# Performance work log

Hardware: AMD Instinct MI355X
Metric: run time of the kernel (lower is better)

## Reference

```python
import jax, jax.numpy as jnp
import numpy as np

B, S, D = 8, 2048, 1024  # batch, seq_len, d_model == output_size


def setup_inputs() -> dict:
    key = jax.random.key(0)
    ks = jax.random.split(key, 10)
    scale = 1.0 / np.sqrt(D)
    return {
        "query": jax.random.normal(ks[0], (B, S, D), jnp.float32),
        "key": jax.random.normal(ks[1], (B, S, D), jnp.float32),
        "value": jax.random.normal(ks[2], (B, S, D), jnp.float32),
        "mask": jax.random.randint(ks[3], (B, S), 0, 2, jnp.int32),
        "Wq": jax.random.uniform(ks[4], (D, D), jnp.float32, -scale, scale),
        "bq": jax.random.uniform(ks[5], (D,), jnp.float32, -scale, scale),
        "Wk": jax.random.uniform(ks[6], (D, D), jnp.float32, -scale, scale),
        "bk": jax.random.uniform(ks[7], (D,), jnp.float32, -scale, scale),
        "Wv": jax.random.uniform(ks[8], (D, D), jnp.float32, -scale, scale),
        "bv": jax.random.uniform(ks[9], (D,), jnp.float32, -scale, scale),
    }


def reference(query, key, value, mask, Wq, bq, Wk, bk, Wv, bv):
    # Linear projections (torch Linear: x @ W.T + b)
    Q = jnp.einsum("bsd,od->bso", query, Wq) + bq
    K = jnp.einsum("bsd,od->bso", key, Wk) + bk
    V = jnp.einsum("bsd,od->bso", value, Wv) + bv
    d_k = K.shape[-1]
    scores = jnp.einsum("bqd,bkd->bqk", Q, K) / jnp.sqrt(jnp.float32(d_k))
    # 2-D mask [B, S_k] -> broadcast over query positions; masked_fill(~mask, -inf)
    m = (mask != 0)[:, None, :]  # [B, 1, S_k]
    scores = jnp.where(m, scores, -jnp.inf)
    weights = jax.nn.softmax(scores, axis=-1)
    # dropout omitted (eval-mode / deterministic baseline)
    out = jnp.einsum("bqk,bkv->bqv", weights, V)
    return out
```

## Files before the change

### kernel.cpp

```cpp
#include <hip/hip_runtime.h>


#define BATCH 8
#define SEQ   2048
#define DM    1024

typedef __bf16 bf16x8 __attribute__((ext_vector_type(8)));
typedef float  f32x4  __attribute__((ext_vector_type(4)));
typedef unsigned short ushort8 __attribute__((ext_vector_type(8)));
typedef unsigned short ushort4v __attribute__((ext_vector_type(4)));

__device__ __forceinline__ unsigned short f2b(float f) {
    __bf16 h = (__bf16)f;
    return __builtin_bit_cast(unsigned short, h);
}

__device__ __forceinline__ void stage_async(const unsigned short* g,
                                            unsigned short* l) {
    __builtin_amdgcn_global_load_lds(
        (const __attribute__((address_space(1))) void*)g,
        (__attribute__((address_space(3))) void*)l, 16, 0, 0);
}

__device__ __forceinline__ void frag_mfma48(const unsigned short* As,
                                            const unsigned short* Bs,
                                            f32x4 acc[4][8], int waveM,
                                            int waveN, int quad, int l16) {
    bf16x8 af[4], bf[8];
#pragma unroll
    for (int i = 0; i < 4; ++i)
        af[i] = *(const bf16x8*)(As + (waveM * 64 + i * 16 + l16) * 32 + quad * 8);
#pragma unroll
    for (int j = 0; j < 8; ++j)
        bf[j] = *(const bf16x8*)(Bs + (waveN * 128 + j * 16 + l16) * 32 + quad * 8);
#pragma unroll
    for (int i = 0; i < 4; ++i)
#pragma unroll
        for (int j = 0; j < 8; ++j)
            acc[i][j] = __builtin_amdgcn_mfma_f32_16x16x32_bf16(
                af[i], bf[j], acc[i][j], 0, 0, 0);
}

__global__ __launch_bounds__(256) void build_idx(
    const int* __restrict__ mask, int* __restrict__ idx,
    int* __restrict__ cnt, int* __restrict__ cntp) {
    const int b = blockIdx.x;
    const int* m = mask + b * SEQ;
    const int t = threadIdx.x;
    __shared__ int sums[256];
    int loc[8], s = 0;
#pragma unroll
    for (int u = 0; u < 8; ++u) { loc[u] = (m[t * 8 + u] != 0); s += loc[u]; }
    sums[t] = s;
    __syncthreads();
    for (int off = 1; off < 256; off <<= 1) {
        int v = (t >= off) ? sums[t - off] : 0;
        __syncthreads();
        sums[t] += v;
        __syncthreads();
    }
    int base = sums[t] - s;
#pragma unroll
    for (int u = 0; u < 8; ++u)
        if (loc[u]) idx[b * SEQ + base++] = t * 8 + u;
    if (t == 255) {
        cnt[b] = sums[255];
        cntp[b] = (sums[255] + 127) & ~127;
    }
}

__global__ void cast_bf16_all(const float* __restrict__ Wq,
                              const float* __restrict__ Wk,
                              const float* __restrict__ Wv,
                              unsigned short* __restrict__ wq,
                              unsigned short* __restrict__ wk,
                              unsigned short* __restrict__ wv) {
    const int p = blockIdx.x >> 9;
    const int lb = blockIdx.x & 511;
    const float* src = (p == 0) ? Wq : (p == 1) ? Wk : Wv;
    unsigned short* dst = (p == 0) ? wq : (p == 1) ? wk : wv;
    int i = lb * blockDim.x + threadIdx.x;
    const f32x4* s4 = (const f32x4*)src;
    f32x4 a = s4[2 * i], b = s4[2 * i + 1];
    ushort8 o;
    o[0] = f2b(a[0]); o[1] = f2b(a[1]); o[2] = f2b(a[2]); o[3] = f2b(a[3]);
    o[4] = f2b(b[0]); o[5] = f2b(b[1]); o[6] = f2b(b[2]); o[7] = f2b(b[3]);
    ((ushort8*)dst)[i] = o;
}

template <bool GATHER, bool TROUT>
__device__ __forceinline__ void proj_body(
    const float* __restrict__ X, const unsigned short* __restrict__ W,
    unsigned short* __restrict__ C, const float* __restrict__ bias,
    const int* __restrict__ idx, const int* __restrict__ cnt,
    const int* __restrict__ cntp, int bz, int mt, int nt,
    unsigned short* As0, unsigned short* As1,
    unsigned short* Bs0, unsigned short* Bs1) {
    const int n0 = nt * 256;
    const int m0 = mt * 128;
    if (GATHER && m0 >= cntp[bz]) return;

    const int tid = threadIdx.x;
    const int wave = tid >> 6, lane = tid & 63;
    const int waveM = wave >> 1, waveN = wave & 1;
    const int quad = lane >> 4, l16 = lane & 15;

    f32x4 acc[4][8] = {};

    const int arow = tid >> 1;
    const int col0 = (tid & 1) * 16;
    const float* rp;
    if (GATHER) {
        const int gm = m0 + arow;
        rp = (gm < cnt[bz])
                 ? X + ((size_t)bz * SEQ + idx[bz * SEQ + gm]) * DM + col0
                 : nullptr;
    } else {
        rp = X + ((size_t)bz * SEQ + m0 + arow) * DM + col0;
    }
    const int lAoff = arow * 32 + col0;

    const int sr = lane >> 2, sc = (lane & 3) * 8;
    const unsigned short* gB = W + (size_t)(n0 + wave * 16 + sr) * DM + sc;
    const int lBoff = (wave * 16 + sr) * 32 + sc;

    const bool haveA = (!GATHER) || (rp != nullptr);

    f32x4 a0 = {}, a1 = {}, a2 = {}, a3 = {};
    if (haveA) {
        const f32x4* p4 = (const f32x4*)rp;
        a0 = p4[0]; a1 = p4[1]; a2 = p4[2]; a3 = p4[3];
    }
#pragma unroll
    for (int c = 0; c < 4; ++c)
        stage_async(gB + (size_t)c * 64 * DM, Bs0 + lBoff + c * 64 * 32);
    {
        ushort8 o0, o1;
        o0[0] = f2b(a0[0]); o0[1] = f2b(a0[1]); o0[2] = f2b(a0[2]); o0[3] = f2b(a0[3]);
        o0[4] = f2b(a1[0]); o0[5] = f2b(a1[1]); o0[6] = f2b(a1[2]); o0[7] = f2b(a1[3]);
        o1[0] = f2b(a2[0]); o1[1] = f2b(a2[1]); o1[2] = f2b(a2[2]); o1[3] = f2b(a2[3]);
        o1[4] = f2b(a3[0]); o1[5] = f2b(a3[1]); o1[6] = f2b(a3[2]); o1[7] = f2b(a3[3]);
        *(ushort8*)(As0 + lAoff) = o0;
        *(ushort8*)(As0 + lAoff + 8) = o1;
    }
    if (haveA) {
        const f32x4* p4 = (const f32x4*)(rp + 32);
        a0 = p4[0]; a1 = p4[1]; a2 = p4[2]; a3 = p4[3];
    }
    __syncthreads();

    int cur = 0;
    for (int kt = 0; kt < DM; kt += 32) {
        const int nx = kt + 32;
        if (nx < DM) {
            unsigned short* Asn = cur ? As0 : As1;
            unsigned short* Bsn = cur ? Bs0 : Bs1;
#pragma unroll
            for (int c = 0; c < 4; ++c)
                stage_async(gB + (size_t)c * 64 * DM + nx,
                            Bsn + lBoff + c * 64 * 32);
            ushort8 o0, o1;
            o0[0] = f2b(a0[0]); o0[1] = f2b(a0[1]); o0[2] = f2b(a0[2]); o0[3] = f2b(a0[3]);
            o0[4] = f2b(a1[0]); o0[5] = f2b(a1[1]); o0[6] = f2b(a1[2]); o0[7] = f2b(a1[3]);
            o1[0] = f2b(a2[0]); o1[1] = f2b(a2[1]); o1[2] = f2b(a2[2]); o1[3] = f2b(a2[3]);
            o1[4] = f2b(a3[0]); o1[5] = f2b(a3[1]); o1[6] = f2b(a3[2]); o1[7] = f2b(a3[3]);
            *(ushort8*)(Asn + lAoff) = o0;
            *(ushort8*)(Asn + lAoff + 8) = o1;
            if (haveA && nx + 32 < DM) {
                const f32x4* p4 = (const f32x4*)(rp + nx + 32);
                a0 = p4[0]; a1 = p4[1]; a2 = p4[2]; a3 = p4[3];
            }
        }
        frag_mfma48(cur ? As1 : As0, cur ? Bs1 : Bs0, acc, waveM, waveN, quad, l16);
        __syncthreads();
        cur ^= 1;
    }

    if (!TROUT) {
        unsigned short* Cb = C + (size_t)bz * SEQ * DM;
#pragma unroll
        for (int i = 0; i < 4; ++i) {
            const int gmb = m0 + waveM * 64 + i * 16 + quad * 4;
#pragma unroll
            for (int j = 0; j < 8; ++j) {
                const int gn = n0 + waveN * 128 + j * 16 + l16;
                const float bv = bias[gn];
#pragma unroll
                for (int r = 0; r < 4; ++r)
                    Cb[(size_t)(gmb + r) * DM + gn] = f2b(acc[i][j][r] + bv);
            }
        }
    } else {
        unsigned short* Cb = C + (size_t)bz * (size_t)DM * SEQ;
#pragma unroll
        for (int i = 0; i < 4; ++i) {
            const int gmb = m0 + waveM * 64 + i * 16 + quad * 4;
#pragma unroll
            for (int j = 0; j < 8; ++j) {
                const int gn = n0 + waveN * 128 + j * 16 + l16;
                const float bv = bias[gn];
                ushort4v o;
#pragma unroll
                for (int r = 0; r < 4; ++r) o[r] = f2b(acc[i][j][r] + bv);
                *(ushort4v*)(Cb + (size_t)gn * SEQ + gmb) = o;
            }
        }
    }
}

__global__ __launch_bounds__(256, 2) void proj_gemm_all(
    const float* __restrict__ q, const float* __restrict__ k,
    const float* __restrict__ v, const unsigned short* __restrict__ wq,
    const unsigned short* __restrict__ wk, const unsigned short* __restrict__ wv,
    unsigned short* __restrict__ Qp, unsigned short* __restrict__ Kc,
    unsigned short* __restrict__ Vt, const float* __restrict__ bq,
    const float* __restrict__ bk, const float* __restrict__ bv,
    const int* __restrict__ idx, const int* __restrict__ cnt,
    const int* __restrict__ cntp) {
    const int l = blockIdx.x + 8 * (blockIdx.y + 16 * blockIdx.z);
    const int p = l >> 9;
    const int bz = l & 7;
    const int t = (l & 511) >> 3;
    const int nt = t & 3, mt = t >> 2;

    __shared__ __align__(16) unsigned short As[2][128 * 32];
    __shared__ __align__(16) unsigned short Bs[2][256 * 32];

    if (p == 0)
        proj_body<false, false>(q, wq, Qp, bq, nullptr, nullptr, nullptr,
                                bz, mt, nt, As[0], As[1], Bs[0], Bs[1]);
    else if (p == 1)
        proj_body<true, false>(k, wk, Kc, bk, idx, cnt, cntp,
                               bz, mt, nt, As[0], As[1], Bs[0], Bs[1]);
    else
        proj_body<true, true>(v, wv, Vt, bv, idx, cnt, cntp,
                              bz, mt, nt, As[0], As[1], Bs[0], Bs[1]);
}

__global__ __launch_bounds__(256, 2) void scores_gemm(
    const unsigned short* __restrict__ Qp, const unsigned short* __restrict__ Kc,
    unsigned short* __restrict__ P, float* __restrict__ rowsum,
    const int* __restrict__ cnt, const int* __restrict__ cntp, float scale) {
    const int l = blockIdx.x + 8 * (blockIdx.y + 16 * blockIdx.z);
    const int bz = l & 7;
    const int i2 = l >> 3;
    const int n0 = (i2 & 7) * 256;
    const int m0 = (i2 >> 3) * 128;
    if (n0 >= cntp[bz]) return;

    const int tid = threadIdx.x;
    const int wave = tid >> 6, lane = tid & 63;
    const int waveM = wave >> 1, waveN = wave & 1;
    const int quad = lane >> 4, l16 = lane & 15;

    __shared__ __align__(16) unsigned short As[2][128 * 32];
    __shared__ __align__(16) unsigned short Bs[2][256 * 32];
    f32x4 acc[4][8] = {};

    const unsigned short* Ag = Qp + (size_t)bz * SEQ * DM;
    const unsigned short* Bg = Kc + (size_t)bz * SEQ * DM;
    const int sr = lane >> 2, sc = (lane & 3) * 8;
    const unsigned short* gA = Ag + (size_t)(m0 + wave * 32 + sr) * DM + sc;
    const unsigned short* gB = Bg + (size_t)(n0 + wave * 16 + sr) * DM + sc;
    const int lAoff = (wave * 32 + sr) * 32 + sc;
    const int lBoff = (wave * 16 + sr) * 32 + sc;

    stage_async(gA, As[0] + lAoff);
    stage_async(gA + 16 * DM, As[0] + lAoff + 16 * 32);
#pragma unroll
    for (int c = 0; c < 4; ++c)
        stage_async(gB + (size_t)c * 64 * DM, Bs[0] + lBoff + c * 64 * 32);
    __syncthreads();

    int cur = 0;
    for (int kt = 0; kt < DM; kt += 32) {
        const int nx = kt + 32;
        if (nx < DM) {
            unsigned short* Asn = cur ? As[0] : As[1];
            unsigned short* Bsn = cur ? Bs[0] : Bs[1];
            stage_async(gA + nx, Asn + lAoff);
            stage_async(gA + nx + 16 * DM, Asn + lAoff + 16 * 32);
#pragma unroll
            for (int c = 0; c < 4; ++c)
                stage_async(gB + (size_t)c * 64 * DM + nx,
                            Bsn + lBoff + c * 64 * 32);
        }
        frag_mfma48(cur ? As[1] : As[0], cur ? Bs[1] : Bs[0], acc,
                    waveM, waveN, quad, l16);
        __syncthreads();
        cur ^= 1;
    }

    unsigned short* Cb = P + (size_t)bz * SEQ * SEQ;
    const int cn = cnt[bz];
#pragma unroll
    for (int i = 0; i < 4; ++i) {
        const int gmb = m0 + waveM * 64 + i * 16 + quad * 4;
        float rpart[4] = {0.f, 0.f, 0.f, 0.f};
#pragma unroll
        for (int j = 0; j < 8; ++j) {
            const int gn = n0 + waveN * 128 + j * 16 + l16;
            const float mv = (gn < cn) ? 1.0f : 0.0f;
#pragma unroll
            for (int r = 0; r < 4; ++r) {
                const float p = mv * __expf(acc[i][j][r] * scale);
                rpart[r] += p;
                Cb[(size_t)(gmb + r) * SEQ + gn] = f2b(p);
            }
        }
#pragma unroll
        for (int r = 0; r < 4; ++r) {
            float s = rpart[r];
            s += __shfl_xor(s, 1, 64);
            s += __shfl_xor(s, 2, 64);
            s += __shfl_xor(s, 4, 64);
            s += __shfl_xor(s, 8, 64);
            if (l16 == 0)
                atomicAdd(&rowsum[bz * SEQ + gmb + r], s);
        }
    }
}

__global__ __launch_bounds__(256, 2) void pv_gemm(
    const unsigned short* __restrict__ P, const unsigned short* __restrict__ Vt,
    float* __restrict__ O, const float* __restrict__ rowsum,
    const int* __restrict__ cntp) {
    const int l = blockIdx.x + 8 * (blockIdx.y + 8 * blockIdx.z);
    const int bz = l & 7;
    const int i2 = l >> 3;
    const int n0 = (i2 & 3) * 256;
    const int m0 = (i2 >> 2) * 128;
    const int kend = cntp[bz];

    const int tid = threadIdx.x;
    const int wave = tid >> 6, lane = tid & 63;
    const int waveM = wave >> 1, waveN = wave & 1;
    const int quad = lane >> 4, l16 = lane & 15;

    __shared__ __align__(16) unsigned short As[2][128 * 32];
    __shared__ __align__(16) unsigned short Bs[2][256 * 32];
    f32x4 acc[4][8] = {};

    const unsigned short* Ag = P + (size_t)bz * SEQ * SEQ;
    const unsigned short* Bg = Vt + (size_t)bz * (size_t)DM * SEQ;
    const int sr = lane >> 2, sc = (lane & 3) * 8;
    const unsigned short* gA = Ag + (size_t)(m0 + wave * 32 + sr) * SEQ + sc;
    const unsigned short* gB = Bg + (size_t)(n0 + wave * 16 + sr) * SEQ + sc;
    const int lAoff = (wave * 32 + sr) * 32 + sc;
    const int lBoff = (wave * 16 + sr) * 32 + sc;

    stage_async(gA, As[0] + lAoff);
    stage_async(gA + 16 * SEQ, As[0] + lAoff + 16 * 32);
#pragma unroll
    for (int c = 0; c < 4; ++c)
        stage_async(gB + (size_t)c * 64 * SEQ, Bs[0] + lBoff + c * 64 * 32);
    __syncthreads();

    int cur = 0;
    for (int kt = 0; kt < kend; kt += 32) {
        const int nx = kt + 32;
        if (nx < kend) {
            unsigned short* Asn = cur ? As[0] : As[1];
            unsigned short* Bsn = cur ? Bs[0] : Bs[1];
            stage_async(gA + nx, Asn + lAoff);
            stage_async(gA + nx + 16 * SEQ, Asn + lAoff + 16 * 32);
#pragma unroll
            for (int c = 0; c < 4; ++c)
                stage_async(gB + (size_t)c * 64 * SEQ + nx,
                            Bsn + lBoff + c * 64 * 32);
        }
        frag_mfma48(cur ? As[1] : As[0], cur ? Bs[1] : Bs[0], acc,
                    waveM, waveN, quad, l16);
        __syncthreads();
        cur ^= 1;
    }

    float* Cb = O + (size_t)bz * SEQ * DM;
#pragma unroll
    for (int i = 0; i < 4; ++i) {
        const int gmb = m0 + waveM * 64 + i * 16 + quad * 4;
        float inv[4];
#pragma unroll
        for (int r = 0; r < 4; ++r)
            inv[r] = 1.0f / rowsum[bz * SEQ + gmb + r];
#pragma unroll
        for (int j = 0; j < 8; ++j) {
            const int gn = n0 + waveN * 128 + j * 16 + l16;
#pragma unroll
            for (int r = 0; r < 4; ++r)
                Cb[(size_t)(gmb + r) * DM + gn] = acc[i][j][r] * inv[r];
        }
    }
}

extern "C" void kernel_launch(void* const* d_in, const int* in_sizes, int n_in,
                              void* d_out, int out_size, void* d_ws, size_t ws_size,
                              hipStream_t stream) {
    const float* query = (const float*)d_in[0];
    const float* key_  = (const float*)d_in[1];
    const float* value = (const float*)d_in[2];
    const int*   mask  = (const int*)d_in[3];
    const float* Wq = (const float*)d_in[4];
    const float* bq = (const float*)d_in[5];
    const float* Wk = (const float*)d_in[6];
    const float* bk = (const float*)d_in[7];
    const float* Wv = (const float*)d_in[8];
    const float* bv = (const float*)d_in[9];
    float* out = (float*)d_out;

    char* ws = (char*)d_ws;
    const size_t MB = 1024 * 1024;
    unsigned short* Qp    = (unsigned short*)(ws);
    unsigned short* Kc    = (unsigned short*)(ws + 32 * MB);
    unsigned short* Vtc   = (unsigned short*)(ws + 64 * MB);
    unsigned short* probs = (unsigned short*)(ws + 96 * MB);
    unsigned short* wq    = (unsigned short*)(ws + 160 * MB);
    unsigned short* wk    = (unsigned short*)(ws + 162 * MB);
    unsigned short* wv    = (unsigned short*)(ws + 164 * MB);
    float* rowsum = (float*)(ws + 166 * MB);
    int*   idx    = (int*)(ws + 166 * MB + 64 * 1024);
    int*   cnt    = (int*)(ws + 166 * MB + 128 * 1024);
    int*   cntp   = (int*)(ws + 166 * MB + 128 * 1024 + 64);

    hipMemsetAsync(rowsum, 0, (size_t)BATCH * SEQ * sizeof(float), stream);
    build_idx<<<BATCH, 256, 0, stream>>>(mask, idx, cnt, cntp);

    cast_bf16_all<<<1536, 256, 0, stream>>>(Wq, Wk, Wv, wq, wk, wv);

    proj_gemm_all<<<dim3(8, 16, 12), dim3(256), 0, stream>>>(
        query, key_, value, wq, wk, wv, Qp, Kc, Vtc, bq, bk, bv,
        idx, cnt, cntp);

    scores_gemm<<<dim3(8, 16, 8), dim3(256), 0, stream>>>(
        Qp, Kc, probs, rowsum, cnt, cntp, 0.03125f);

    pv_gemm<<<dim3(8, 8, 8), dim3(256), 0, stream>>>(
        probs, Vtc, out, rowsum, cntp);
}
```

Before: 435.7 us.

## Pre-gather and cast K/V to bf16, use async LDS loads with 128x128 tiles

Adds a separate kernel that gathers the unmasked K and V rows and casts them to bf16 in workspace buffers. The K/V projection can then stage both operands straight into LDS with async global_load_lds instead of converting in registers. Projection tiles shrink from 128x256 to 128x128 with a 64-deep K step per barrier pair, which doubles the grid and drops the occupancy hint. The cost is an extra read-write pass over K/V in bf16, and the loop no longer overlaps the next load with compute across iterations.

Result: no change. 427.3 us (-1.9%).

```diff
diff --git a/kernel.cpp b/kernel.cpp
--- a/kernel.cpp
+++ b/kernel.cpp
@@ -20,6 +20,25 @@
     __builtin_amdgcn_global_load_lds(
         (const __attribute__((address_space(1))) void*)g,
         (__attribute__((address_space(3))) void*)l, 16, 0, 0);
+}
+
+__device__ __forceinline__ void frag_mfma(const unsigned short* As,
+                                          const unsigned short* Bs,
+                                          f32x4 acc[4][4], int waveM, int waveN,
+                                          int quad, int l16) {
+    bf16x8 af[4], bf[4];
+#pragma unroll
+    for (int i = 0; i < 4; ++i)
+        af[i] = *(const bf16x8*)(As + (waveM * 64 + i * 16 + l16) * 32 + quad * 8);
+#pragma unroll
+    for (int j = 0; j < 4; ++j)
+        bf[j] = *(const bf16x8*)(Bs + (waveN * 64 + j * 16 + l16) * 32 + quad * 8);
+#pragma unroll
+    for (int i = 0; i < 4; ++i)
+#pragma unroll
+        for (int j = 0; j < 4; ++j)
+            acc[i][j] = __builtin_amdgcn_mfma_f32_16x16x32_bf16(
+                af[i], bf[j], acc[i][j], 0, 0, 0);
 }
 
 __device__ __forceinline__ void frag_mfma48(const unsigned short* As,
@@ -88,153 +107,200 @@
     ((ushort8*)dst)[i] = o;
 }
 
-template <bool GATHER, bool TROUT>
-__device__ __forceinline__ void proj_body(
-    const float* __restrict__ X, const unsigned short* __restrict__ W,
+__global__ __launch_bounds__(256) void cast_kv(
+    const float* __restrict__ key, const float* __restrict__ value,
+    unsigned short* __restrict__ Kg, unsigned short* __restrict__ Vg,
+    const int* __restrict__ idx, const int* __restrict__ cnt,
+    const int* __restrict__ cntp) {
+    const int b = blockIdx.x;
+    const int p = b >> 13;
+    const int r = b & 8191;
+    const int bz = r >> 10;
+    const int rowpair = r & 1023;
+    const int t = threadIdx.x;
+    const int row = rowpair * 2 + (t >> 7);
+    if (row >= cntp[bz]) return;
+    const int col0 = (t & 127) * 8;
+    const float* src = p ? value : key;
+    unsigned short* dst = p ? Vg : Kg;
+    ushort8 o = {};
+    if (row < cnt[bz]) {
+        const int srow = idx[bz * SEQ + row];
+        const f32x4* s4 =
+            (const f32x4*)(src + ((size_t)bz * SEQ + srow) * DM + col0);
+        f32x4 a = s4[0], c = s4[1];
+        o[0] = f2b(a[0]); o[1] = f2b(a[1]); o[2] = f2b(a[2]); o[3] = f2b(a[3]);
+        o[4] = f2b(c[0]); o[5] = f2b(c[1]); o[6] = f2b(c[2]); o[7] = f2b(c[3]);
+    }
+    *(ushort8*)(dst + ((size_t)bz * SEQ + row) * DM + col0) = o;
+}
+
+template <bool TROUT>
+__device__ __forceinline__ void proj_epilogue(
+    f32x4 acc[4][4], unsigned short* __restrict__ C,
+    const float* __restrict__ bias, int bz, int m0, int n0,
+    int waveM, int waveN, int quad, int l16) {
+    if (!TROUT) {
+        unsigned short* Cb = C + (size_t)bz * SEQ * DM;
+#pragma unroll
+        for (int i = 0; i < 4; ++i) {
+            const int gmb = m0 + waveM * 64 + i * 16 + quad * 4;
+#pragma unroll
+            for (int j = 0; j < 4; ++j) {
+                const int gn = n0 + waveN * 64 + j * 16 + l16;
+                const float bv = bias[gn];
+#pragma unroll
+                for (int r = 0; r < 4; ++r)
+                    Cb[(size_t)(gmb + r) * DM + gn] = f2b(acc[i][j][r] + bv);
+            }
+        }
+    } else {
+        unsigned short* Cb = C + (size_t)bz * (size_t)DM * SEQ;
+#pragma unroll
+        for (int i = 0; i < 4; ++i) {
+            const int gmb = m0 + waveM * 64 + i * 16 + quad * 4;
+#pragma unroll
+            for (int j = 0; j < 4; ++j) {
+                const int gn = n0 + waveN * 64 + j * 16 + l16;
+                const float bv = bias[gn];
+                ushort4v o;
+#pragma unroll
+                for (int r = 0; r < 4; ++r) o[r] = f2b(acc[i][j][r] + bv);
+                *(ushort4v*)(Cb + (size_t)gn * SEQ + gmb) = o;
+            }
+        }
+    }
+}
+
+template <bool TROUT>
+__device__ __forceinline__ void proj_pure_body(
+    const unsigned short* __restrict__ Xg, const unsigned short* __restrict__ W,
     unsigned short* __restrict__ C, const float* __restrict__ bias,
-    const int* __restrict__ idx, const int* __restrict__ cnt,
-    const int* __restrict__ cntp, int bz, int mt, int nt,
-    unsigned short* As0, unsigned short* As1,
-    unsigned short* Bs0, unsigned short* Bs1) {
-    const int n0 = nt * 256;
-    const int m0 = mt * 128;
-    if (GATHER && m0 >= cntp[bz]) return;
+    const int* __restrict__ cntp, int bz, int i2,
+    unsigned short (*As)[128 * 32], unsigned short (*Bs)[128 * 32]) {
+    const int n0 = (i2 & 7) * 128;
+    const int m0 = (i2 >> 3) * 128;
+    if (m0 >= cntp[bz]) return;
 
     const int tid = threadIdx.x;
     const int wave = tid >> 6, lane = tid & 63;
     const int waveM = wave >> 1, waveN = wave & 1;
     const int quad = lane >> 4, l16 = lane & 15;
 
-    f32x4 acc[4][8] = {};
+    f32x4 acc[4][4] = {};
+
+    const int sr = lane >> 2, sc = (lane & 3) * 8;
+    const unsigned short* gA =
+        Xg + (size_t)bz * SEQ * DM + (size_t)(m0 + wave * 32 + sr) * DM + sc;
+    const unsigned short* gB = W + (size_t)(n0 + wave * 32 + sr) * DM + sc;
+    const int loff = (wave * 32 + sr) * 32 + sc;
+
+    for (int kt = 0; kt < DM; kt += 64) {
+#pragma unroll
+        for (int ph = 0; ph < 2; ++ph) {
+            const int ko = kt + ph * 32;
+            stage_async(gA + ko, As[ph] + loff);
+            stage_async(gA + ko + 16 * DM, As[ph] + loff + 16 * 32);
+            stage_async(gB + ko, Bs[ph] + loff);
+            stage_async(gB + ko + 16 * DM, Bs[ph] + loff + 16 * 32);
+        }
+        __syncthreads();
+        frag_mfma(As[0], Bs[0], acc, waveM, waveN, quad, l16);
+        frag_mfma(As[1], Bs[1], acc, waveM, waveN, quad, l16);
+        __syncthreads();
+    }
+    proj_epilogue<TROUT>(acc, C, bias, bz, m0, n0, waveM, waveN, quad, l16);
+}
+
+__device__ __forceinline__ void proj_q_body(
+    const float* __restrict__ X, const unsigned short* __restrict__ W,
+    unsigned short* __restrict__ C, const float* __restrict__ bias,
+    int bz, int i2,
+    unsigned short (*As)[128 * 32], unsigned short (*Bs)[128 * 32]) {
+    const int n0 = (i2 & 7) * 128;
+    const int m0 = (i2 >> 3) * 128;
+
+    const int tid = threadIdx.x;
+    const int wave = tid >> 6, lane = tid & 63;
+    const int waveM = wave >> 1, waveN = wave & 1;
+    const int quad = lane >> 4, l16 = lane & 15;
+
+    f32x4 acc[4][4] = {};
 
     const int arow = tid >> 1;
     const int col0 = (tid & 1) * 16;
-    const float* rp;
-    if (GATHER) {
-        const int gm = m0 + arow;
-        rp = (gm < cnt[bz])
-                 ? X + ((size_t)bz * SEQ + idx[bz * SEQ + gm]) * DM + col0
-                 : nullptr;
-    } else {
-        rp = X + ((size_t)bz * SEQ + m0 + arow) * DM + col0;
-    }
+    const float* rp = X + ((size_t)bz * SEQ + m0 + arow) * DM + col0;
     const int lAoff = arow * 32 + col0;
 
     const int sr = lane >> 2, sc = (lane & 3) * 8;
-    const unsigned short* gB = W + (size_t)(n0 + wave * 16 + sr) * DM + sc;
-    const int lBoff = (wave * 16 + sr) * 32 + sc;
-
-    const bool haveA = (!GATHER) || (rp != nullptr);
-
-    f32x4 a0 = {}, a1 = {}, a2 = {}, a3 = {};
-    if (haveA) {
-        const f32x4* p4 = (const f32x4*)rp;
-        a0 = p4[0]; a1 = p4[1]; a2 = p4[2]; a3 = p4[3];
-    }
-#pragma unroll
-    for (int c = 0; c < 4; ++c)
-        stage_async(gB + (size_t)c * 64 * DM, Bs0 + lBoff + c * 64 * 32);
+    const unsigned short* gB = W + (size_t)(n0 + wave * 32 + sr) * DM + sc;
+    const int lBoff = (wave * 32 + sr) * 32 + sc;
+
+    f32x4 a0, a1, a2, a3, a4, a5, a6, a7;
     {
-        ushort8 o0, o1;
+        const f32x4* p0 = (const f32x4*)(rp);
+        const f32x4* p1 = (const f32x4*)(rp + 32);
+        a0 = p0[0]; a1 = p0[1]; a2 = p0[2]; a3 = p0[3];
+        a4 = p1[0]; a5 = p1[1]; a6 = p1[2]; a7 = p1[3];
+    }
+
+    for (int kt = 0; kt < DM; kt += 64) {
+#pragma unroll
+        for (int ph = 0; ph < 2; ++ph) {
+            const int ko = kt + ph * 32;
+            stage_async(gB + ko, Bs[ph] + lBoff);
+            stage_async(gB + ko + 16 * DM, Bs[ph] + lBoff + 16 * 32);
+        }
+        ushort8 o0, o1, o2, o3;
         o0[0] = f2b(a0[0]); o0[1] = f2b(a0[1]); o0[2] = f2b(a0[2]); o0[3] = f2b(a0[3]);
         o0[4] = f2b(a1[0]); o0[5] = f2b(a1[1]); o0[6] = f2b(a1[2]); o0[7] = f2b(a1[3]);
         o1[0] = f2b(a2[0]); o1[1] = f2b(a2[1]); o1[2] = f2b(a2[2]); o1[3] = f2b(a2[3]);
         o1[4] = f2b(a3[0]); o1[5] = f2b(a3[1]); o1[6] = f2b(a3[2]); o1[7] = f2b(a3[3]);
-        *(ushort8*)(As0 + lAoff) = o0;
-        *(ushort8*)(As0 + lAoff + 8) = o1;
-    }
-    if (haveA) {
-        const f32x4* p4 = (const f32x4*)(rp + 32);
-        a0 = p4[0]; a1 = p4[1]; a2 = p4[2]; a3 = p4[3];
-    }
-    __syncthreads();
-
-    int cur = 0;
-    for (int kt = 0; kt < DM; kt += 32) {
-        const int nx = kt + 32;
-        if (nx < DM) {
-            unsigned short* Asn = cur ? As0 : As1;
-            unsigned short* Bsn = cur ? Bs0 : Bs1;
-#pragma unroll
-            for (int c = 0; c < 4; ++c)
-                stage_async(gB + (size_t)c * 64 * DM + nx,
-                            Bsn + lBoff + c * 64 * 32);
-            ushort8 o0, o1;
-            o0[0] = f2b(a0[0]); o0[1] = f2b(a0[1]); o0[2] = f2b(a0[2]); o0[3] = f2b(a0[3]);
-            o0[4] = f2b(a1[0]); o0[5] = f2b(a1[1]); o0[6] = f2b(a1[2]); o0[7] = f2b(a1[3]);
-            o1[0] = f2b(a2[0]); o1[1] = f2b(a2[1]); o1[2] = f2b(a2[2]); o1[3] = f2b(a2[3]);
-            o1[4] = f2b(a3[0]); o1[5] = f2b(a3[1]); o1[6] = f2b(a3[2]); o1[7] = f2b(a3[3]);
-            *(ushort8*)(Asn + lAoff) = o0;
-            *(ushort8*)(Asn + lAoff + 8) = o1;
-            if (haveA && nx + 32 < DM) {
-                const f32x4* p4 = (const f32x4*)(rp + nx + 32);
-                a0 = p4[0]; a1 = p4[1]; a2 = p4[2]; a3 = p4[3];
-            }
-        }
-        frag_mfma48(cur ? As1 : As0, cur ? Bs1 : Bs0, acc, waveM, waveN, quad, l16);
-        __syncthreads();
-        cur ^= 1;
-    }
-
-    if (!TROUT) {
-        unsigned short* Cb = C + (size_t)bz * SEQ * DM;
-#pragma unroll
-        for (int i = 0; i < 4; ++i) {
-            const int gmb = m0 + waveM * 64 + i * 16 + quad * 4;
-#pragma unroll
-            for (int j = 0; j < 8; ++j) {
-                const int gn = n0 + waveN * 128 + j * 16 + l16;
-                const float bv = bias[gn];
-#pragma unroll
-                for (int r = 0; r < 4; ++r)
-                    Cb[(size_t)(gmb + r) * DM + gn] = f2b(acc[i][j][r] + bv);
-            }
-        }
-    } else {
-        unsigned short* Cb = C + (size_t)bz * (size_t)DM * SEQ;
-#pragma unroll
-        for (int i = 0; i < 4; ++i) {
-            const int gmb = m0 + waveM * 64 + i * 16 + quad * 4;
-#pragma unroll
-            for (int j = 0; j < 8; ++j) {
-                const int gn = n0 + waveN * 128 + j * 16 + l16;
-                const float bv = bias[gn];
-                ushort4v o;
-#pragma unroll
-                for (int r = 0; r < 4; ++r) o[r] = f2b(acc[i][j][r] + bv);
-                *(ushort4v*)(Cb + (size_t)gn * SEQ + gmb) = o;
-            }
-        }
-    }
-}
-
-__global__ __launch_bounds__(256, 2) void proj_gemm_all(
-    const float* __restrict__ q, const float* __restrict__ k,
-    const float* __restrict__ v, const unsigned short* __restrict__ wq,
-    const unsigned short* __restrict__ wk, const unsigned short* __restrict__ wv,
+        o2[0] = f2b(a4[0]); o2[1] = f2b(a4[1]); o2[2] = f2b(a4[2]); o2[3] = f2b(a4[3]);
+        o2[4] = f2b(a5[0]); o2[5] = f2b(a5[1]); o2[6] = f2b(a5[2]); o2[7] = f2b(a5[3]);
+        o3[0] = f2b(a6[0]); o3[1] = f2b(a6[1]); o3[2] = f2b(a6[2]); o3[3] = f2b(a6[3]);
+        o3[4] = f2b(a7[0]); o3[5] = f2b(a7[1]); o3[6] = f2b(a7[2]); o3[7] = f2b(a7[3]);
+        *(ushort8*)(As[0] + lAoff) = o0;
+        *(ushort8*)(As[0] + lAoff + 8) = o1;
+        *(ushort8*)(As[1] + lAoff) = o2;
+        *(ushort8*)(As[1] + lAoff + 8) = o3;
+        if (kt + 64 < DM) {
+            const f32x4* p0 = (const f32x4*)(rp + kt + 64);
+            const f32x4* p1 = (const f32x4*)(rp + kt + 96);
+            a0 = p0[0]; a1 = p0[1]; a2 = p0[2]; a3 = p0[3];
+            a4 = p1[0]; a5 = p1[1]; a6 = p1[2]; a7 = p1[3];
+        }
+        __syncthreads();
+        frag_mfma(As[0], Bs[0], acc, waveM, waveN, quad, l16);
+        frag_mfma(As[1], Bs[1], acc, waveM, waveN, quad, l16);
+        __syncthreads();
+    }
+    proj_epilogue<false>(acc, C, bias, bz, m0, n0, waveM, waveN, quad, l16);
+}
+
+__global__ __launch_bounds__(256) void proj_gemm_all(
+    const float* __restrict__ q, const unsigned short* __restrict__ Kg,
+    const unsigned short* __restrict__ Vg,
+    const unsigned short* __restrict__ wq, const unsigned short* __restrict__ wk,
+    const unsigned short* __restrict__ wv,
     unsigned short* __restrict__ Qp, unsigned short* __restrict__ Kc,
     unsigned short* __restrict__ Vt, const float* __restrict__ bq,
     const float* __restrict__ bk, const float* __restrict__ bv,
-    const int* __restrict__ idx, const int* __restrict__ cnt,
     const int* __restrict__ cntp) {
     const int l = blockIdx.x + 8 * (blockIdx.y + 16 * blockIdx.z);
-    const int p = l >> 9;
+    const int p = l >> 10;
     const int bz = l & 7;
-    const int t = (l & 511) >> 3;
-    const int nt = t & 3, mt = t >> 2;
+    const int i2 = (l & 1023) >> 3;
 
     __shared__ __align__(16) unsigned short As[2][128 * 32];
-    __shared__ __align__(16) unsigned short Bs[2][256 * 32];
+    __shared__ __align__(16) unsigned short Bs[2][128 * 32];
 
     if (p == 0)
-        proj_body<false, false>(q, wq, Qp, bq, nullptr, nullptr, nullptr,
-                                bz, mt, nt, As[0], As[1], Bs[0], Bs[1]);
+        proj_q_body(q, wq, Qp, bq, bz, i2, As, Bs);
     else if (p == 1)
-        proj_body<true, false>(k, wk, Kc, bk, idx, cnt, cntp,
-                               bz, mt, nt, As[0], As[1], Bs[0], Bs[1]);
+        proj_pure_body<false>(Kg, wk, Kc, bk, cntp, bz, i2, As, Bs);
     else
-        proj_body<true, true>(v, wv, Vt, bv, idx, cnt, cntp,
-                              bz, mt, nt, As[0], As[1], Bs[0], Bs[1]);
+        proj_pure_body<true>(Vg, wv, Vt, bv, cntp, bz, i2, As, Bs);
 }
 
 __global__ __launch_bounds__(256, 2) void scores_gemm(
@@ -414,6 +480,8 @@
     unsigned short* Kc    = (unsigned short*)(ws + 32 * MB);
     unsigned short* Vtc   = (unsigned short*)(ws + 64 * MB);
     unsigned short* probs = (unsigned short*)(ws + 96 * MB);
+    unsigned short* Kg    = probs;
+    unsigned short* Vg    = (unsigned short*)(ws + 128 * MB);
     unsigned short* wq    = (unsigned short*)(ws + 160 * MB);
     unsigned short* wk    = (unsigned short*)(ws + 162 * MB);
     unsigned short* wv    = (unsigned short*)(ws + 164 * MB);
@@ -426,10 +494,10 @@
     build_idx<<<BATCH, 256, 0, stream>>>(mask, idx, cnt, cntp);
 
     cast_bf16_all<<<1536, 256, 0, stream>>>(Wq, Wk, Wv, wq, wk, wv);
-
-    proj_gemm_all<<<dim3(8, 16, 12), dim3(256), 0, stream>>>(
-        query, key_, value, wq, wk, wv, Qp, Kc, Vtc, bq, bk, bv,
-        idx, cnt, cntp);
+    cast_kv<<<16384, 256, 0, stream>>>(key_, value, Kg, Vg, idx, cnt, cntp);
+
+    proj_gemm_all<<<dim3(8, 16, 24), dim3(256), 0, stream>>>(
+        query, Kg, Vg, wq, wk, wv, Qp, Kc, Vtc, bq, bk, bv, cntp);
 
     scores_gemm<<<dim3(8, 16, 8), dim3(256), 0, stream>>>(
         Qp, Kc, probs, rowsum, cnt, cntp, 0.03125f);
```
